# Optimization experiments

Measured on AMD Instinct MI355X. Metric: run time of the kernel, lower is better.

## Reference

```python
import jax, jax.numpy as jnp
import numpy as np

N_NODES = 50000
N_EDGES = 800000
IN_DIM, HID, N_CLS = 128, 128, 64


def setup_inputs() -> dict:
    key = jax.random.key(0)
    ks = jax.random.split(key, 10)
    x = jax.random.normal(ks[0], (N_NODES, IN_DIM), dtype=jnp.float32)
    src = jax.random.randint(ks[1], (N_EDGES,), 0, N_NODES, dtype=jnp.int32)
    dst = jax.random.randint(ks[2], (N_EDGES,), 0, N_NODES, dtype=jnp.int32)
    def lin(k, fi, fo):
        s = 1.0 / np.sqrt(fi)
        return jax.random.uniform(k, (fi, fo), jnp.float32, -s, s)
    # layer dims: 128->128, 128->128, 128->64 (num_layers=2 -> 3 SAGEConv layers)
    params = {
        'W_self0': lin(ks[3], IN_DIM, HID), 'W_neigh0': lin(ks[4], IN_DIM, HID),
        'b0': jnp.zeros((HID,), jnp.float32),
        'W_self1': lin(ks[5], HID, HID), 'W_neigh1': lin(ks[6], HID, HID),
        'b1': jnp.zeros((HID,), jnp.float32),
        'W_self2': lin(ks[7], HID, N_CLS), 'W_neigh2': lin(ks[8], HID, N_CLS),
        'b2': jnp.zeros((N_CLS,), jnp.float32),
    }
    return {'x': x, 'src': src, 'dst': dst, **params}


def _sage_layer(h, src, dst, W_self, W_neigh, b):
    # mean aggregator: gather source features, segment-sum into dst, divide by in-degree
    msg = h[src]                                                   # [E, d]
    agg = jax.ops.segment_sum(msg, dst, num_segments=N_NODES)      # [N, d]
    deg = jax.ops.segment_sum(jnp.ones((src.shape[0],), h.dtype), dst,
                              num_segments=N_NODES)
    h_neigh = agg / jnp.maximum(deg, 1.0)[:, None]
    return h @ W_self + h_neigh @ W_neigh + b


def reference(x, src, dst, W_self0, W_neigh0, b0, W_self1, W_neigh1, b1,
              W_self2, W_neigh2, b2):
    h = _sage_layer(x, src, dst, W_self0, W_neigh0, b0)
    h = jax.nn.relu(h)
    h = _sage_layer(h, src, dst, W_self1, W_neigh1, b1)
    h = jax.nn.relu(h)
    h = _sage_layer(h, src, dst, W_self2, W_neigh2, b2)
    return h
```

## Files before the change

### kernel.cpp

```cpp
#include <hip/hip_runtime.h>
#include <hip/hip_bf16.h>


#define NFEAT 128
#define SLOTS 64

typedef __attribute__((ext_vector_type(8))) short short8;
typedef __attribute__((ext_vector_type(4))) float floatx4;

__device__ __forceinline__ float bf_lo(unsigned u) { return __uint_as_float(u << 16); }
__device__ __forceinline__ float bf_hi(unsigned u) { return __uint_as_float(u & 0xffff0000u); }
__device__ __forceinline__ ushort f2bf(float f) {
    __hip_bfloat16 h = __float2bfloat16(f);
    return *(ushort*)&h;
}
__device__ __forceinline__ unsigned pack2(float a, float b) {
    return (unsigned)f2bf(a) | ((unsigned)f2bf(b) << 16);
}


__global__ __launch_bounds__(256) void k_prep(
    const int* __restrict__ dst, const int* __restrict__ src,
    int* __restrict__ deg, ushort* __restrict__ csr,
    int E, int NN,
    const float* __restrict__ X, ushort* __restrict__ X16, int n2,
    const float* __restrict__ Ws0, const float* __restrict__ Wn0,
    const float* __restrict__ Ws1, const float* __restrict__ Wn1,
    const float* __restrict__ Ws2, const float* __restrict__ Wn2,
    ushort* __restrict__ Wt0, ushort* __restrict__ Wt1, ushort* __restrict__ Wt2,
    int e8b, int cvtb) {
    int b = blockIdx.x, t = threadIdx.x;
    if (b < e8b) {
        int base = (b * 256 + t) * 8;
        if (base + 8 <= E) {
            int4 da = *(const int4*)(dst + base);
            int4 db = *(const int4*)(dst + base + 4);
            int4 sa = *(const int4*)(src + base);
            int4 sb = *(const int4*)(src + base + 4);
            int r0 = atomicAdd(&deg[da.x], 1);
            int r1 = atomicAdd(&deg[da.y], 1);
            int r2 = atomicAdd(&deg[da.z], 1);
            int r3 = atomicAdd(&deg[da.w], 1);
            int r4 = atomicAdd(&deg[db.x], 1);
            int r5 = atomicAdd(&deg[db.y], 1);
            int r6 = atomicAdd(&deg[db.z], 1);
            int r7 = atomicAdd(&deg[db.w], 1);
            if (r0 < SLOTS) csr[(da.x << 6) + r0] = (ushort)sa.x;
            if (r1 < SLOTS) csr[(da.y << 6) + r1] = (ushort)sa.y;
            if (r2 < SLOTS) csr[(da.z << 6) + r2] = (ushort)sa.z;
            if (r3 < SLOTS) csr[(da.w << 6) + r3] = (ushort)sa.w;
            if (r4 < SLOTS) csr[(db.x << 6) + r4] = (ushort)sb.x;
            if (r5 < SLOTS) csr[(db.y << 6) + r5] = (ushort)sb.y;
            if (r6 < SLOTS) csr[(db.z << 6) + r6] = (ushort)sb.z;
            if (r7 < SLOTS) csr[(db.w << 6) + r7] = (ushort)sb.w;
        } else {
            for (int e = base; e < E; ++e) {
                int d = dst[e];
                int r = atomicAdd(&deg[d], 1);
                if (r < SLOTS) csr[(d << 6) + r] = (ushort)src[e];
            }
        }
    } else if (b < e8b + cvtb) {
        int i = (b - e8b) * 256 + t;
        if (i < n2) {
            float2 v = ((const float2*)X)[i];
            ((unsigned*)X16)[i] = pack2(v.x, v.y);
        }
    } else {
        int idx = (b - e8b - cvtb) * 256 + t;
        if (idx < 32768) {
            int n = idx >> 8, k = idx & 255;
            Wt0[idx] = f2bf(k < 128 ? Ws0[k * 128 + n] : Wn0[(k - 128) * 128 + n]);
        } else if (idx < 65536) {
            int l = idx - 32768, n = l >> 8, k = l & 255;
            Wt1[l] = f2bf(k < 128 ? Ws1[k * 128 + n] : Wn1[(k - 128) * 128 + n]);
        } else if (idx < 81920) {
            int l = idx - 65536, n = l >> 8, k = l & 255;
            Wt2[l] = f2bf(k < 128 ? Ws2[k * 64 + n] : Wn2[(k - 128) * 64 + n]);
        }
    }
}


template <int FEAT, int MODE>
__device__ __forceinline__ void agg_body(int vbid, int nb, int t,
    const ushort* __restrict__ H, const int* __restrict__ deg,
    const ushort* __restrict__ csr, void* __restrict__ outp, int NN) {
    constexpr int LPR = FEAT / 8;
    constexpr int EPG = 64 / LPR;
    constexpr int NS = 8;
    int lane = t & 63, wid = t >> 6;
    int sub = lane / LPR, fl = lane % LPR;
    int wstr = nb * 4;
    int node = vbid * 4 + wid;

    int d_cur = 0;
    int s_cur[NS];
    if (node < NN) {
        d_cur = deg[node];
        const ushort* slot = csr + (node << 6);
#pragma unroll
        for (int k = 0; k < NS; ++k) s_cur[k] = slot[k * EPG + sub];
    }

    while (node < NN) {
        int nnode = node + wstr;
        int d_nxt = 0;
        int s_nxt[NS];
        if (nnode < NN) {
            d_nxt = deg[nnode];
            const ushort* slot2 = csr + (nnode << 6);
#pragma unroll
            for (int k = 0; k < NS; ++k) s_nxt[k] = slot2[k * EPG + sub];
        }

        int dd = d_cur;
        int d = (dd < SLOTS) ? dd : SLOTS;
        float acc[8] = {};
        uint4 v[NS];
#pragma unroll
        for (int k = 0; k < NS; ++k) {
            int e = k * EPG + sub;
            v[k] = make_uint4(0, 0, 0, 0);
            if (e < d) v[k] = *(const uint4*)(H + (size_t)s_cur[k] * FEAT + fl * 8);
        }
#pragma unroll
        for (int k = 0; k < NS; ++k) {
            acc[0] += bf_lo(v[k].x); acc[1] += bf_hi(v[k].x);
            acc[2] += bf_lo(v[k].y); acc[3] += bf_hi(v[k].y);
            acc[4] += bf_lo(v[k].z); acc[5] += bf_hi(v[k].z);
            acc[6] += bf_lo(v[k].w); acc[7] += bf_hi(v[k].w);
        }
        if constexpr (NS * EPG < SLOTS) {
            if (d > NS * EPG) {
                const ushort* slot = csr + (node << 6);
                for (int e = NS * EPG + sub; e < d; e += EPG) {
                    int r = slot[e];
                    uint4 vv = *(const uint4*)(H + (size_t)r * FEAT + fl * 8);
                    acc[0] += bf_lo(vv.x); acc[1] += bf_hi(vv.x);
                    acc[2] += bf_lo(vv.y); acc[3] += bf_hi(vv.y);
                    acc[4] += bf_lo(vv.z); acc[5] += bf_hi(vv.z);
                    acc[6] += bf_lo(vv.w); acc[7] += bf_hi(vv.w);
                }
            }
        }
#pragma unroll
        for (int off = LPR; off < 64; off <<= 1)
#pragma unroll
            for (int i = 0; i < 8; ++i) acc[i] += __shfl_xor(acc[i], off, 64);
        if (sub == 0) {
            float inv = (dd > 0) ? 1.0f / (float)dd : 0.0f;
            if constexpr (MODE == 0) {
                unsigned u[4];
#pragma unroll
                for (int i = 0; i < 4; ++i)
                    u[i] = pack2(acc[2 * i] * inv, acc[2 * i + 1] * inv);
                *(uint4*)((ushort*)outp + (size_t)node * FEAT + fl * 8) =
                    make_uint4(u[0], u[1], u[2], u[3]);
            } else {
                float* O = (float*)outp;
                size_t b = (size_t)node * FEAT + fl * 8;
#pragma unroll
                for (int i = 0; i < 8; ++i) O[b + i] += acc[i] * inv;
            }
        }
        node = nnode;
        d_cur = d_nxt;
#pragma unroll
        for (int k = 0; k < NS; ++k) s_cur[k] = s_nxt[k];
    }
}

__global__ __launch_bounds__(256) void k_agg128(
    const ushort* __restrict__ H, const int* __restrict__ deg,
    const ushort* __restrict__ csr, void* __restrict__ outp, int NN) {
    agg_body<128, 0>(blockIdx.x, gridDim.x, threadIdx.x, H, deg, csr, outp, NN);
}

__global__ __launch_bounds__(256) void k_aggacc(
    const ushort* __restrict__ G2, const int* __restrict__ deg,
    const ushort* __restrict__ csr, float* __restrict__ out, int NN) {
    agg_body<64, 2>(blockIdx.x, gridDim.x, threadIdx.x, G2, deg, csr, out, NN);
}


template <int BM, int BN, int NKB, bool SPLIT, bool OUT_BF16>
__device__ __forceinline__ void gemm_body(int bid, int t,
    const ushort* __restrict__ Hs, const ushort* __restrict__ Ag,
    const ushort* __restrict__ Wt, int ldw, const float* __restrict__ bias,
    void* __restrict__ Cout, int M, int relu) {
    constexpr int NW = BN / 64;
    constexpr int NTHR = 2 * NW * 64;
    constexpr int MT = BM / 32;
    constexpr int LDA = 40;
    __shared__ ushort Asl[BM * LDA];
    __shared__ ushort Bsl[BN * LDA];

    int lane = t & 63;
    int wid = t >> 6;
    int wm = wid & 1, wn = wid >> 1;
    int l15 = lane & 15, quad = lane >> 4;
    int m0 = bid * BM;

    floatx4 acc[MT][4] = {};

    for (int kb = 0; kb < NKB; ++kb) {
        const ushort* Asrc;
        int kOff;
        if constexpr (SPLIT) {
            Asrc = (kb < NKB / 2) ? Hs : Ag;
            kOff = (kb & (NKB / 2 - 1)) * 32;
        } else {
            Asrc = Hs;
            kOff = kb * 32;
        }
        __syncthreads();
#pragma unroll
        for (int id = t; id < BM * 4; id += NTHR) {
            int r = id >> 2, p = id & 3;
            uint4 v = make_uint4(0, 0, 0, 0);
            if (m0 + r < M) v = *(const uint4*)(Asrc + (size_t)(m0 + r) * NFEAT + kOff + p * 8);
            *(uint4*)(&Asl[r * LDA + p * 8]) = v;
        }
#pragma unroll
        for (int id = t; id < BN * 4; id += NTHR) {
            int r = id >> 2, p = id & 3;
            uint4 v = *(const uint4*)(Wt + (size_t)r * ldw + kb * 32 + p * 8);
            *(uint4*)(&Bsl[r * LDA + p * 8]) = v;
        }
        __syncthreads();

        short8 a[MT], b[4];
#pragma unroll
        for (int mt = 0; mt < MT; ++mt)
            a[mt] = *(const short8*)(&Asl[(wm * (MT * 16) + mt * 16 + l15) * LDA + quad * 8]);
#pragma unroll
        for (int nt = 0; nt < 4; ++nt)
            b[nt] = *(const short8*)(&Bsl[(wn * 64 + nt * 16 + l15) * LDA + quad * 8]);
#pragma unroll
        for (int mt = 0; mt < MT; ++mt)
#pragma unroll
            for (int nt = 0; nt < 4; ++nt)
                acc[mt][nt] = __builtin_amdgcn_mfma_f32_16x16x32_bf16(a[mt], b[nt], acc[mt][nt], 0, 0, 0);
    }

#pragma unroll
    for (int mt = 0; mt < MT; ++mt) {
        int mbase = m0 + wm * (MT * 16) + mt * 16 + quad * 4;
#pragma unroll
        for (int nt = 0; nt < 4; ++nt) {
            int col = wn * 64 + nt * 16 + l15;
            float bv = bias ? bias[col] : 0.0f;
#pragma unroll
            for (int r = 0; r < 4; ++r) {
                int m = mbase + r;
                if (m < M) {
                    float v = acc[mt][nt][r] + bv;
                    if (relu) v = fmaxf(v, 0.f);
                    if constexpr (OUT_BF16) {
                        ((unsigned short*)Cout)[(size_t)m * BN + col] = f2bf(v);
                    } else {
                        ((float*)Cout)[(size_t)m * BN + col] = v;
                    }
                }
            }
        }
    }
}

__global__ __launch_bounds__(256) void k_gemm(
    const ushort* __restrict__ Hs, const ushort* __restrict__ Ag,
    const ushort* __restrict__ Wt, const float* __restrict__ bias,
    ushort* __restrict__ Hout, int M) {
    gemm_body<64, 128, 8, true, true>(blockIdx.x, threadIdx.x,
                                      Hs, Ag, Wt, 256, bias, Hout, M, 1);
}

__global__ __launch_bounds__(128) void k_d7(
    const ushort* __restrict__ Hb, const ushort* __restrict__ Wt2,
    const float* __restrict__ b2, ushort* __restrict__ G2,
    float* __restrict__ out, int M, int pb) {
    if ((int)blockIdx.x < pb)
        gemm_body<64, 64, 4, false, true>(blockIdx.x, threadIdx.x,
                                          Hb, nullptr, Wt2 + 128, 256, nullptr, G2, M, 0);
    else
        gemm_body<64, 64, 4, false, false>(blockIdx.x - pb, threadIdx.x,
                                           Hb, nullptr, Wt2, 256, b2, out, M, 0);
}


static inline size_t align_up(size_t x) { return (x + 255) & ~(size_t)255; }

extern "C" void kernel_launch(void* const* d_in, const int* in_sizes, int n_in,
                              void* d_out, int out_size, void* d_ws, size_t ws_size,
                              hipStream_t stream) {
    const float* x   = (const float*)d_in[0];
    const int*   src = (const int*)d_in[1];
    const int*   dst = (const int*)d_in[2];
    const float* Ws0 = (const float*)d_in[3];
    const float* Wn0 = (const float*)d_in[4];
    const float* b0  = (const float*)d_in[5];
    const float* Ws1 = (const float*)d_in[6];
    const float* Wn1 = (const float*)d_in[7];
    const float* b1  = (const float*)d_in[8];
    const float* Ws2 = (const float*)d_in[9];
    const float* Wn2 = (const float*)d_in[10];
    const float* b2  = (const float*)d_in[11];
    float* out = (float*)d_out;

    const int NN = in_sizes[0] / NFEAT;
    const int E  = in_sizes[1];

    char* w = (char*)d_ws;
    ushort* X16  = (ushort*)w; w += align_up((size_t)NN * NFEAT * 2);
    ushort* Ha   = (ushort*)w; w += align_up((size_t)NN * NFEAT * 2);
    ushort* Hb   = (ushort*)w; w += align_up((size_t)NN * NFEAT * 2);
    ushort* AGG  = (ushort*)w; w += align_up((size_t)NN * NFEAT * 2);
    ushort* Wt0  = (ushort*)w; w += align_up((size_t)128 * 256 * 2);
    ushort* Wt1  = (ushort*)w; w += align_up((size_t)128 * 256 * 2);
    ushort* Wt2  = (ushort*)w; w += align_up((size_t)64 * 256 * 2);
    int* deg     = (int*)w;    w += align_up((size_t)NN * 4);
    ushort* csr  = (ushort*)w; w += align_up((size_t)NN * SLOTS * 2);

    ushort* G2  = X16;

    hipMemsetAsync(deg, 0, (size_t)NN * 4, stream);

    const int e8b  = (E / 8 + 255) / 256;
    const int n2   = NN * NFEAT / 2;
    const int cvtb = (n2 + 255) / 256;
    const int wb   = (81920 + 255) / 256;
    const int gm   = (NN + 63) / 64;
    const int agb  = 2048;

    k_prep<<<e8b + cvtb + wb, 256, 0, stream>>>(
        dst, src, deg, csr, E, NN, x, X16, n2,
        Ws0, Wn0, Ws1, Wn1, Ws2, Wn2, Wt0, Wt1, Wt2, e8b, cvtb);

    k_agg128<<<agb, 256, 0, stream>>>(X16, deg, csr, AGG, NN);
    k_gemm<<<gm, 256, 0, stream>>>(X16, AGG, Wt0, b0, Ha, NN);

    k_agg128<<<agb, 256, 0, stream>>>(Ha, deg, csr, AGG, NN);
    k_gemm<<<gm, 256, 0, stream>>>(Ha, AGG, Wt1, b1, Hb, NN);

    k_d7<<<gm * 2, 128, 0, stream>>>(Hb, Wt2, b2, G2, out, NN, gm);
    k_aggacc<<<agb, 256, 0, stream>>>(G2, deg, csr, out, NN);
}
```

Baseline: 264.7 us.

## Precompute layer-0 self GEMM in prep kernel and pad degree counters

Computes X@W_self0 inside the prep kernel as extra blocks writing fp32 S0, so the first layer GEMM only multiplies the aggregated neighbours (K=128) and adds S0 in its epilogue. This moves half of layer 0's GEMM off the critical path, where it can overlap with the atomic CSR build. Separately, degree counters are spread to one per 64 bytes to reduce atomic contention. The cost is an extra 25MB fp32 write and read of S0, a 16x larger memset for deg, and the fallback depends on workspace size.

Measured after the change: 275.5 us. 4.1% more time.

```diff
diff --git a/kernel.cpp b/kernel.cpp
--- a/kernel.cpp
+++ b/kernel.cpp
@@ -16,6 +16,74 @@
 }
 __device__ __forceinline__ unsigned pack2(float a, float b) {
     return (unsigned)f2bf(a) | ((unsigned)f2bf(b) << 16);
+}
+
+
+__device__ __forceinline__ void selfgemm0_body(int bid, int t,
+    const float* __restrict__ X, const float* __restrict__ Ws0,
+    float* __restrict__ S0, int M) {
+    constexpr int LDA = 40;
+    __shared__ ushort Asl[64 * LDA];
+    __shared__ ushort Bsl[128 * LDA];
+    int lane = t & 63, wid = t >> 6;
+    int wm = wid & 1, wn = wid >> 1;
+    int l15 = lane & 15, quad = lane >> 4;
+    int m0 = bid * 64;
+    floatx4 acc[2][4] = {};
+
+    for (int kb = 0; kb < 4; ++kb) {
+        __syncthreads();
+#pragma unroll
+        for (int id = t; id < 64 * 4; id += 256) {
+            int r = id >> 2, p = id & 3;
+            uint4 u = make_uint4(0, 0, 0, 0);
+            if (m0 + r < M) {
+                const float* xp = X + (size_t)(m0 + r) * 128 + kb * 32 + p * 8;
+                float4 v0 = *(const float4*)(xp);
+                float4 v1 = *(const float4*)(xp + 4);
+                u = make_uint4(pack2(v0.x, v0.y), pack2(v0.z, v0.w),
+                               pack2(v1.x, v1.y), pack2(v1.z, v1.w));
+            }
+            *(uint4*)(&Asl[r * LDA + p * 8]) = u;
+        }
+#pragma unroll
+        for (int id = t; id < 128 * 4; id += 256) {
+            int r = id >> 2, p = id & 3;
+            const float* wp = Ws0 + (size_t)(kb * 32 + p * 8) * 128 + r;
+            float f0 = wp[0 * 128], f1 = wp[1 * 128], f2 = wp[2 * 128], f3 = wp[3 * 128];
+            float f4 = wp[4 * 128], f5 = wp[5 * 128], f6 = wp[6 * 128], f7 = wp[7 * 128];
+            *(uint4*)(&Bsl[r * LDA + p * 8]) =
+                make_uint4(pack2(f0, f1), pack2(f2, f3), pack2(f4, f5), pack2(f6, f7));
+        }
+        __syncthreads();
+
+        short8 a[2], b[4];
+#pragma unroll
+        for (int mt = 0; mt < 2; ++mt)
+            a[mt] = *(const short8*)(&Asl[(wm * 32 + mt * 16 + l15) * LDA + quad * 8]);
+#pragma unroll
+        for (int nt = 0; nt < 4; ++nt)
+            b[nt] = *(const short8*)(&Bsl[(wn * 64 + nt * 16 + l15) * LDA + quad * 8]);
+#pragma unroll
+        for (int mt = 0; mt < 2; ++mt)
+#pragma unroll
+            for (int nt = 0; nt < 4; ++nt)
+                acc[mt][nt] = __builtin_amdgcn_mfma_f32_16x16x32_bf16(a[mt], b[nt], acc[mt][nt], 0, 0, 0);
+    }
+
+#pragma unroll
+    for (int mt = 0; mt < 2; ++mt) {
+        int mbase = m0 + wm * 32 + mt * 16 + quad * 4;
+#pragma unroll
+        for (int nt = 0; nt < 4; ++nt) {
+            int col = wn * 64 + nt * 16 + l15;
+#pragma unroll
+            for (int r = 0; r < 4; ++r) {
+                int m = mbase + r;
+                if (m < M) S0[(size_t)m * 128 + col] = acc[mt][nt][r];
+            }
+        }
+    }
 }
 
 
@@ -28,7 +96,8 @@
     const float* __restrict__ Ws1, const float* __restrict__ Wn1,
     const float* __restrict__ Ws2, const float* __restrict__ Wn2,
     ushort* __restrict__ Wt0, ushort* __restrict__ Wt1, ushort* __restrict__ Wt2,
-    int e8b, int cvtb) {
+    float* __restrict__ S0,
+    int e8b, int cvtb, int wb) {
     int b = blockIdx.x, t = threadIdx.x;
     if (b < e8b) {
         int base = (b * 256 + t) * 8;
@@ -37,14 +106,14 @@
             int4 db = *(const int4*)(dst + base + 4);
             int4 sa = *(const int4*)(src + base);
             int4 sb = *(const int4*)(src + base + 4);
-            int r0 = atomicAdd(&deg[da.x], 1);
-            int r1 = atomicAdd(&deg[da.y], 1);
-            int r2 = atomicAdd(&deg[da.z], 1);
-            int r3 = atomicAdd(&deg[da.w], 1);
-            int r4 = atomicAdd(&deg[db.x], 1);
-            int r5 = atomicAdd(&deg[db.y], 1);
-            int r6 = atomicAdd(&deg[db.z], 1);
-            int r7 = atomicAdd(&deg[db.w], 1);
+            int r0 = atomicAdd(&deg[da.x << 4], 1);
+            int r1 = atomicAdd(&deg[da.y << 4], 1);
+            int r2 = atomicAdd(&deg[da.z << 4], 1);
+            int r3 = atomicAdd(&deg[da.w << 4], 1);
+            int r4 = atomicAdd(&deg[db.x << 4], 1);
+            int r5 = atomicAdd(&deg[db.y << 4], 1);
+            int r6 = atomicAdd(&deg[db.z << 4], 1);
+            int r7 = atomicAdd(&deg[db.w << 4], 1);
             if (r0 < SLOTS) csr[(da.x << 6) + r0] = (ushort)sa.x;
             if (r1 < SLOTS) csr[(da.y << 6) + r1] = (ushort)sa.y;
             if (r2 < SLOTS) csr[(da.z << 6) + r2] = (ushort)sa.z;
@@ -56,7 +125,7 @@
         } else {
             for (int e = base; e < E; ++e) {
                 int d = dst[e];
-                int r = atomicAdd(&deg[d], 1);
+                int r = atomicAdd(&deg[d << 4], 1);
                 if (r < SLOTS) csr[(d << 6) + r] = (ushort)src[e];
             }
         }
@@ -66,7 +135,7 @@
             float2 v = ((const float2*)X)[i];
             ((unsigned*)X16)[i] = pack2(v.x, v.y);
         }
-    } else {
+    } else if (b < e8b + cvtb + wb) {
         int idx = (b - e8b - cvtb) * 256 + t;
         if (idx < 32768) {
             int n = idx >> 8, k = idx & 255;
@@ -78,6 +147,8 @@
             int l = idx - 65536, n = l >> 8, k = l & 255;
             Wt2[l] = f2bf(k < 128 ? Ws2[k * 64 + n] : Wn2[(k - 128) * 64 + n]);
         }
+    } else {
+        selfgemm0_body(b - e8b - cvtb - wb, t, X, Ws0, S0, NN);
     }
 }
 
@@ -97,7 +168,7 @@
     int d_cur = 0;
     int s_cur[NS];
     if (node < NN) {
-        d_cur = deg[node];
+        d_cur = deg[node << 4];
         const ushort* slot = csr + (node << 6);
 #pragma unroll
         for (int k = 0; k < NS; ++k) s_cur[k] = slot[k * EPG + sub];
@@ -108,7 +179,7 @@
         int d_nxt = 0;
         int s_nxt[NS];
         if (nnode < NN) {
-            d_nxt = deg[nnode];
+            d_nxt = deg[nnode << 4];
             const ushort* slot2 = csr + (nnode << 6);
 #pragma unroll
             for (int k = 0; k < NS; ++k) s_nxt[k] = slot2[k * EPG + sub];
@@ -184,10 +255,11 @@
 }
 
 
-template <int BM, int BN, int NKB, bool SPLIT, bool OUT_BF16>
+template <int BM, int BN, int NKB, bool SPLIT, bool OUT_BF16, bool ADDS0>
 __device__ __forceinline__ void gemm_body(int bid, int t,
     const ushort* __restrict__ Hs, const ushort* __restrict__ Ag,
     const ushort* __restrict__ Wt, int ldw, const float* __restrict__ bias,
+    const float* __restrict__ Sadd,
     void* __restrict__ Cout, int M, int relu) {
     constexpr int NW = BN / 64;
     constexpr int NTHR = 2 * NW * 64;
@@ -256,6 +328,7 @@
                 int m = mbase + r;
                 if (m < M) {
                     float v = acc[mt][nt][r] + bv;
+                    if constexpr (ADDS0) v += Sadd[(size_t)m * BN + col];
                     if (relu) v = fmaxf(v, 0.f);
                     if constexpr (OUT_BF16) {
                         ((unsigned short*)Cout)[(size_t)m * BN + col] = f2bf(v);
@@ -268,12 +341,20 @@
     }
 }
 
+__global__ __launch_bounds__(256) void k_gemm_ns(
+    const ushort* __restrict__ Ag, const ushort* __restrict__ Wt,
+    const float* __restrict__ bias, const float* __restrict__ S0,
+    ushort* __restrict__ Hout, int M) {
+    gemm_body<64, 128, 4, false, true, true>(blockIdx.x, threadIdx.x,
+                                             Ag, nullptr, Wt + 128, 256, bias, S0, Hout, M, 1);
+}
+
 __global__ __launch_bounds__(256) void k_gemm(
     const ushort* __restrict__ Hs, const ushort* __restrict__ Ag,
     const ushort* __restrict__ Wt, const float* __restrict__ bias,
     ushort* __restrict__ Hout, int M) {
-    gemm_body<64, 128, 8, true, true>(blockIdx.x, threadIdx.x,
-                                      Hs, Ag, Wt, 256, bias, Hout, M, 1);
+    gemm_body<64, 128, 8, true, true, false>(blockIdx.x, threadIdx.x,
+                                             Hs, Ag, Wt, 256, bias, nullptr, Hout, M, 1);
 }
 
 __global__ __launch_bounds__(128) void k_d7(
@@ -281,11 +362,11 @@
     const float* __restrict__ b2, ushort* __restrict__ G2,
     float* __restrict__ out, int M, int pb) {
     if ((int)blockIdx.x < pb)
-        gemm_body<64, 64, 4, false, true>(blockIdx.x, threadIdx.x,
-                                          Hb, nullptr, Wt2 + 128, 256, nullptr, G2, M, 0);
+        gemm_body<64, 64, 4, false, true, false>(blockIdx.x, threadIdx.x,
+                                                 Hb, nullptr, Wt2 + 128, 256, nullptr, nullptr, G2, M, 0);
     else
-        gemm_body<64, 64, 4, false, false>(blockIdx.x - pb, threadIdx.x,
-                                           Hb, nullptr, Wt2, 256, b2, out, M, 0);
+        gemm_body<64, 64, 4, false, false, false>(blockIdx.x - pb, threadIdx.x,
+                                                  Hb, nullptr, Wt2, 256, b2, nullptr, out, M, 0);
 }
 
 
@@ -319,12 +400,15 @@
     ushort* Wt0  = (ushort*)w; w += align_up((size_t)128 * 256 * 2);
     ushort* Wt1  = (ushort*)w; w += align_up((size_t)128 * 256 * 2);
     ushort* Wt2  = (ushort*)w; w += align_up((size_t)64 * 256 * 2);
-    int* deg     = (int*)w;    w += align_up((size_t)NN * 4);
+    int* deg     = (int*)w;    w += align_up((size_t)NN * 16 * 4);
     ushort* csr  = (ushort*)w; w += align_up((size_t)NN * SLOTS * 2);
+    float* S0    = (float*)w;  w += align_up((size_t)NN * NFEAT * 4);
 
     ushort* G2  = X16;
 
-    hipMemsetAsync(deg, 0, (size_t)NN * 4, stream);
+    const bool fold = ((size_t)(w - (char*)d_ws) <= ws_size);
+
+    hipMemsetAsync(deg, 0, (size_t)NN * 16 * 4, stream);
 
     const int e8b  = (E / 8 + 255) / 256;
     const int n2   = NN * NFEAT / 2;
@@ -333,12 +417,15 @@
     const int gm   = (NN + 63) / 64;
     const int agb  = 2048;
 
-    k_prep<<<e8b + cvtb + wb, 256, 0, stream>>>(
+    k_prep<<<e8b + cvtb + wb + (fold ? gm : 0), 256, 0, stream>>>(
         dst, src, deg, csr, E, NN, x, X16, n2,
-        Ws0, Wn0, Ws1, Wn1, Ws2, Wn2, Wt0, Wt1, Wt2, e8b, cvtb);
+        Ws0, Wn0, Ws1, Wn1, Ws2, Wn2, Wt0, Wt1, Wt2, S0, e8b, cvtb, wb);
 
     k_agg128<<<agb, 256, 0, stream>>>(X16, deg, csr, AGG, NN);
-    k_gemm<<<gm, 256, 0, stream>>>(X16, AGG, Wt0, b0, Ha, NN);
+    if (fold)
+        k_gemm_ns<<<gm, 256, 0, stream>>>(AGG, Wt0, b0, S0, Ha, NN);
+    else
+        k_gemm<<<gm, 256, 0, stream>>>(X16, AGG, Wt0, b0, Ha, NN);
 
     k_agg128<<<agb, 256, 0, stream>>>(Ha, deg, csr, AGG, NN);
     k_gemm<<<gm, 256, 0, stream>>>(Ha, AGG, Wt1, b1, Hb, NN);
```
